# Kernel optimization log

Measured on AMD Instinct MI355X. Metric: run time of the kernel, lower is better.

The kernel has to match this reference:

```python
import math
import jax, jax.numpy as jnp
import numpy as np

B, S, D, H = 4, 2048, 1024, 16
HD = D // H  # head_dim = 64
EPS = 1e-6
LOG2_E = 1.442695041


def setup_inputs() -> dict:
    key = jax.random.key(0)
    ks = jax.random.split(key, 8)
    return {
        "inputs_q": jax.random.normal(ks[0], (B, S, D), dtype=jnp.float32),
        "Wq": jax.random.normal(ks[1], (D, D), dtype=jnp.float32) * 0.02,
        "Wk": jax.random.normal(ks[2], (D, D), dtype=jnp.float32) * 0.02,
        "Wv": jax.random.normal(ks[3], (D, D), dtype=jnp.float32) * 0.02,
        "Wo": jax.random.normal(ks[4], (D, D), dtype=jnp.float32) * 0.02,
        "q_ln_scale": jnp.ones((HD,), dtype=jnp.float32),
        "k_ln_scale": jnp.ones((HD,), dtype=jnp.float32),
        "per_dim_scale": jax.random.normal(ks[5], (HD,), dtype=jnp.float32) * 0.1,
        "patch_mask": jnp.zeros((B, S), dtype=bool),
    }


def _rope(x, position):
    # x: [B, S, H, HD], position: [B, S]
    half = HD // 2
    fraction = 2.0 * jnp.arange(half, dtype=jnp.float32) / HD
    timescale = 1.0 * (10000.0 / 1.0) ** fraction            # [half]
    sinusoid = position[:, :, None, None].astype(jnp.float32) / timescale[None, None, None, :]
    sin, cos = jnp.sin(sinusoid), jnp.cos(sinusoid)
    first, second = jnp.split(x, 2, axis=-1)
    return jnp.concatenate([first * cos - second * sin,
                            second * cos + first * sin], axis=-1)


def _rms_norm(x, scale):
    var = jnp.mean(jnp.square(x), axis=-1, keepdims=True)
    return x * jax.lax.rsqrt(var + EPS) * scale


def reference(inputs_q, Wq, Wk, Wv, Wo, q_ln_scale, k_ln_scale, per_dim_scale, patch_mask):
    b, s, d = inputs_q.shape
    # QKV projections (nn.Linear, no bias): y = x @ W.T
    q = (inputs_q @ Wq.T).reshape(b, s, H, HD)
    k = (inputs_q @ Wk.T).reshape(b, s, H, HD)
    v = (inputs_q @ Wv.T).reshape(b, s, H, HD)

    num_masked = jnp.sum(patch_mask.astype(jnp.int32), axis=-1)  # [B]
    # decode_cache=None => next_index = 0
    position = jnp.arange(s, dtype=jnp.int32)[None, :] - num_masked[:, None]  # [B, S]

    q = _rope(q, position)
    k = _rope(k, position)

    q = _rms_norm(q, q_ln_scale)
    k = _rms_norm(k, k_ln_scale)

    # per-dim scale
    q = q * (LOG2_E / math.sqrt(HD) * jax.nn.softplus(per_dim_scale))

    # causal + prefix-padding mask: [B, 1, S, S]
    q_idx = jnp.arange(s)[None, None, :, None]
    kv_idx = jnp.arange(s)[None, None, None, :]
    mask = (q_idx >= kv_idx) & (kv_idx >= num_masked[:, None, None, None])

    scores = jnp.einsum("bqhd,bkhd->bhqk", q, k)
    neg = -jnp.finfo(scores.dtype).max / 2
    scores = jnp.where(mask, scores, neg)
    attn = jax.nn.softmax(scores, axis=-1)
    x = jnp.einsum("bhqk,bkhd->bqhd", attn, v).reshape(b, s, d)
    return x @ Wo.T
```

## Files before the change

### kernel.cpp

```cpp
#include <hip/hip_runtime.h>
#include <cstdint>
#include <cstddef>

#define BB 4
#define SS 2048
#define DD 1024
#define HH 16

typedef __bf16 bf16;
typedef __bf16 bf16x8 __attribute__((ext_vector_type(8)));
typedef __bf16 bf16x4 __attribute__((ext_vector_type(4)));
typedef float f32x4 __attribute__((ext_vector_type(4)));
typedef unsigned int u32;

typedef __attribute__((address_space(1))) const void* as1_cvoid;
typedef __attribute__((address_space(3))) void* as3_void;

__device__ __forceinline__ void gload_lds16(const void* g, void* l) {
  __builtin_amdgcn_global_load_lds((as1_cvoid)g, (as3_void)l, 16, 0, 0);
}

__global__ void mask_count_kernel(const unsigned char* __restrict__ mask, int* __restrict__ nm) {
  int wid = threadIdx.x >> 6, lane = threadIdx.x & 63;
  if (wid >= BB) return;
  int s = 0;
  for (int i = lane; i < SS; i += 64) s += (mask[wid * SS + i] != 0) ? 1 : 0;
#pragma unroll
  for (int m = 1; m < 64; m <<= 1) s += __shfl_xor(s, m);
  if (lane == 0) nm[wid] = s;
}

__global__ void cvt_kernel(const float* __restrict__ src, bf16* __restrict__ dst, int n4) {
  int stride = gridDim.x * blockDim.x;
  for (int i = blockIdx.x * blockDim.x + threadIdx.x; i < n4; i += stride) {
    float4 v = ((const float4*)src)[i];
    bf16x4 o;
    o[0] = (bf16)v.x; o[1] = (bf16)v.y; o[2] = (bf16)v.z; o[3] = (bf16)v.w;
    ((bf16x4*)dst)[i] = o;
  }
}

__global__ void sincos_table_kernel(const int* __restrict__ nm, float2* __restrict__ tbl) {
  int g = blockIdx.x * 256 + threadIdx.x;
  int j = g & 31;
  int idx = g >> 5;
  int b = idx >> 11, s = idx & 2047;
  int pos = s - nm[b];
  float inv_ts = __expf((float)j * (-9.210340371976184f / 32.0f));
  float sn, cs;
  sincosf((float)pos * inv_ts, &sn, &cs);
  tbl[g] = make_float2(cs, sn);
}

__global__ void __launch_bounds__(256) gemm_qkv_kernel(
    const bf16* __restrict__ A, const bf16* __restrict__ Wq, const bf16* __restrict__ Wk,
    const bf16* __restrict__ Wv, const float* __restrict__ qls, const float* __restrict__ kls,
    const float* __restrict__ pds, const float2* __restrict__ tbl,
    bf16* __restrict__ Qp, bf16* __restrict__ Kp, bf16* __restrict__ Vt) {
  __shared__ __align__(16) char smem[4 * 64 * 72 * 2];
  bf16* Ab = (bf16*)smem;
  bf16* Bb = (bf16*)(smem + 8192);
  const int tid = threadIdx.x;
  const int wid = tid >> 6, lane = tid & 63;
  const int lr = lane & 15, lg = lane >> 4;
  const int K = DD;
  const int nx = 24;
  const int cpx = gridDim.x >> 3;
  const int lid = (blockIdx.x & 7) * cpx + (blockIdx.x >> 3);
  const int m0 = (lid / nx) * 128;
  const int ntile = lid % nx;
  const int which = ntile >> 3;
  const int n0 = (ntile & 7) * 128;
  const bf16* Bm = which == 0 ? Wq : (which == 1 ? Wk : Wv);
  const int wm = (wid >> 1) * 64, wn = (wid & 1) * 64;
  f32x4 acc[4][4] = {};
  for (int k0 = 0; k0 < K; k0 += 32) {
    __syncthreads();
#pragma unroll
    for (int i = 0; i < 2; ++i) {
      int o = (wid * 2 + i) * 1024 + lane * 16;
      int row = o >> 6;
      int ke = (o & 63) >> 1;
      gload_lds16(A + (size_t)(m0 + row) * K + k0 + ke, (char*)Ab + o);
      gload_lds16(Bm + (size_t)(n0 + row) * K + k0 + ke, (char*)Bb + o);
    }
    __syncthreads();
    bf16x8 af[4], bf_[4];
#pragma unroll
    for (int i = 0; i < 4; ++i) af[i] = *(const bf16x8*)&Ab[(wm + i * 16 + lr) * 32 + lg * 8];
#pragma unroll
    for (int j = 0; j < 4; ++j) bf_[j] = *(const bf16x8*)&Bb[(wn + j * 16 + lr) * 32 + lg * 8];
#pragma unroll
    for (int i = 0; i < 4; ++i)
#pragma unroll
      for (int j = 0; j < 4; ++j)
        acc[i][j] = __builtin_amdgcn_mfma_f32_16x16x32_bf16(af[i], bf_[j], acc[i][j], 0, 0, 0);
  }
  const int b = m0 >> 11;
  const int s0g = m0 & 2047;
  const int hq = n0 >> 6;
  if (which < 2) {
    float scj[4];
#pragma unroll
    for (int j = 0; j < 4; ++j) {
      int d = j * 16 + lr;
      scj[j] = (which == 0) ? qls[d] * 0.26017112262570096f * log1pf(__expf(pds[d]))
                            : kls[d];
    }
    bf16* Out = which == 0 ? Qp : Kp;
    const int h = hq + (wn >> 6);
    const size_t base = (size_t)(b * 16 + h) * SS;
#pragma unroll
    for (int i = 0; i < 4; ++i)
#pragma unroll
      for (int r = 0; r < 4; ++r) {
        int srow = s0g + wm + i * 16 + lg * 4 + r;
        const float2* trow = tbl + ((size_t)(b * SS + srow) << 5);
        float2 t0 = trow[lr], t1 = trow[16 + lr];
        float a0 = acc[i][0][r], a1 = acc[i][1][r], a2 = acc[i][2][r], a3 = acc[i][3][r];
        float n0_ = a0 * t0.x - a2 * t0.y;
        float n2_ = a2 * t0.x + a0 * t0.y;
        float n1_ = a1 * t1.x - a3 * t1.y;
        float n3_ = a3 * t1.x + a1 * t1.y;
        float ssum = n0_ * n0_ + n1_ * n1_ + n2_ * n2_ + n3_ * n3_;
        ssum += __shfl_xor(ssum, 1);
        ssum += __shfl_xor(ssum, 2);
        ssum += __shfl_xor(ssum, 4);
        ssum += __shfl_xor(ssum, 8);
        float rinv = rsqrtf(ssum * (1.0f / 64.0f) + 1e-6f);
        bf16* orow = Out + (base + srow) * 64;
        orow[lr]      = (bf16)(n0_ * rinv * scj[0]);
        orow[16 + lr] = (bf16)(n1_ * rinv * scj[1]);
        orow[32 + lr] = (bf16)(n2_ * rinv * scj[2]);
        orow[48 + lr] = (bf16)(n3_ * rinv * scj[3]);
      }
  } else {
    __syncthreads();
    bf16* tw = (bf16*)smem + wid * 64 * 72;
#pragma unroll
    for (int i = 0; i < 4; ++i)
#pragma unroll
      for (int j = 0; j < 4; ++j)
#pragma unroll
        for (int r = 0; r < 4; ++r)
          tw[(j * 16 + lr) * 72 + i * 16 + lg * 4 + r] = (bf16)acc[i][j][r];
    __syncthreads();
    int d = tid >> 2, sc = (tid & 3) * 16;
#pragma unroll
    for (int w = 0; w < 4; ++w) {
      int rh = w >> 1, hh = w & 1;
      const bf16* ts = (const bf16*)smem + w * 64 * 72 + d * 72 + sc;
      bf16x8 v0 = *(const bf16x8*)ts;
      bf16x8 v1 = *(const bf16x8*)(ts + 8);
      size_t vo = ((size_t)((b * 16 + hq + hh) * 64 + d)) * SS + s0g + rh * 64 + sc;
      *(bf16x8*)(Vt + vo) = v0;
      *(bf16x8*)(Vt + vo + 8) = v1;
    }
  }
}

__global__ void __launch_bounds__(256) gemm_bt_kernel(const bf16* __restrict__ A,
                                                      const bf16* __restrict__ Bm,
                                                      float* __restrict__ Cout,
                                                      int M, int N, int K) {
  __shared__ bf16 Ab[128 * 32];
  __shared__ bf16 Bb[128 * 32];
  const int tid = threadIdx.x;
  const int wid = tid >> 6, lane = tid & 63;
  const int lr = lane & 15, lg = lane >> 4;
  const int nx = N >> 7;
  const int cpx = gridDim.x >> 3;
  const int lid = (blockIdx.x & 7) * cpx + (blockIdx.x >> 3);
  const int m0 = (lid / nx) * 128, n0 = (lid % nx) * 128;
  const int wm = (wid >> 1) * 64, wn = (wid & 1) * 64;
  f32x4 acc[4][4] = {};
  for (int k0 = 0; k0 < K; k0 += 32) {
    __syncthreads();
#pragma unroll
    for (int i = 0; i < 2; ++i) {
      int o = (wid * 2 + i) * 1024 + lane * 16;
      int row = o >> 6;
      int ke = (o & 63) >> 1;
      gload_lds16(A + (size_t)(m0 + row) * K + k0 + ke, (char*)Ab + o);
      gload_lds16(Bm + (size_t)(n0 + row) * K + k0 + ke, (char*)Bb + o);
    }
    __syncthreads();
    bf16x8 af[4], bf_[4];
#pragma unroll
    for (int i = 0; i < 4; ++i) af[i] = *(const bf16x8*)&Ab[(wm + i * 16 + lr) * 32 + lg * 8];
#pragma unroll
    for (int j = 0; j < 4; ++j) bf_[j] = *(const bf16x8*)&Bb[(wn + j * 16 + lr) * 32 + lg * 8];
#pragma unroll
    for (int i = 0; i < 4; ++i)
#pragma unroll
      for (int j = 0; j < 4; ++j)
        acc[i][j] = __builtin_amdgcn_mfma_f32_16x16x32_bf16(af[i], bf_[j], acc[i][j], 0, 0, 0);
  }
#pragma unroll
  for (int i = 0; i < 4; ++i)
#pragma unroll
    for (int j = 0; j < 4; ++j)
#pragma unroll
      for (int r = 0; r < 4; ++r) {
        int row = m0 + wm + i * 16 + lg * 4 + r;
        int col = n0 + wn + j * 16 + lr;
        Cout[(size_t)row * N + col] = acc[i][j][r];
      }
}

__global__ void __launch_bounds__(256, 2) flash_kernel(
    const bf16* __restrict__ Qp, const bf16* __restrict__ Kp, const bf16* __restrict__ Vt,
    bf16* __restrict__ O, const int* __restrict__ nm) {
  __shared__ bf16 Kb[2][64 * 64];
  __shared__ bf16 Vb[64 * 64];
  __shared__ u32 Pl[4][16][36];
  const int bh = blockIdx.x & 63;
  const int px = blockIdx.x >> 6;
  const int xA = 31 - px, xB = px;
  const int b = bh >> 4, h = bh & 15;
  const int tid = threadIdx.x;
  const int wid = tid >> 6, lane = tid & 63;
  const int lr = lane & 15, lg = lane >> 4;
  const int nmb = nm[b];
  const int wqA = xA * 64 + wid * 16;
  const int wqB = xB * 64 + wid * 16;
  const int nt = xA + 1;

  bf16x8 qfA[2], qfB[2];
#pragma unroll
  for (int kh = 0; kh < 2; ++kh) {
    qfA[kh] = *(const bf16x8*)(Qp + ((size_t)bh * SS + wqA + lr) * 64 + kh * 32 + lg * 8);
    qfB[kh] = *(const bf16x8*)(Qp + ((size_t)bh * SS + wqB + lr) * 64 + kh * 32 + lg * 8);
  }

  float mA = -1e30f, lA = 0.f, mB = -1e30f, lB = 0.f;
  f32x4 oA[4] = {}, oB[4] = {};

  auto STAGE_K = [&](int bi, int t) {
    const int kv0 = t * 64;
#pragma unroll
    for (int i = 0; i < 2; ++i) {
      int o = i * 4096 + tid * 16;
      int row = o >> 7;
      int c16 = ((o >> 4) & 7) ^ (row & 7);
      gload_lds16(Kp + ((size_t)bh * SS + kv0 + row) * 64 + c16 * 8, (char*)Kb[bi] + o);
    }
  };
  auto STAGE_V = [&](int t) {
    const int kv0 = t * 64;
#pragma unroll
    for (int i = 0; i < 2; ++i) {
      int o = i * 4096 + tid * 16;
      int row = o >> 7;
      int c16 = ((o >> 4) & 7) ^ (row & 7);
      gload_lds16(Vt + ((size_t)bh * 64 + row) * SS + kv0 + c16 * 8, (char*)Vb + o);
    }
  };

  STAGE_K(0, 0);
  STAGE_V(0);
  __syncthreads();
  int buf = 0;
  for (int t = 0; t < nt; ++t) {
    const int kv0 = t * 64;
    if (t + 1 < nt) STAGE_K(buf ^ 1, t + 1);
    const bool actB = (t <= xB);
    bf16x8 pbA[2], pbB[2];
    f32x4 sA[4], sB[4];

    __builtin_amdgcn_s_setprio(1);
#pragma unroll
    for (int j = 0; j < 4; ++j) {
      int row = j * 16 + lr;
      const char* kbase = (const char*)Kb[buf] + row * 128;
      bf16x8 kf0 = *(const bf16x8*)(kbase + ((lg ^ (row & 7)) << 4));
      bf16x8 kf1 = *(const bf16x8*)(kbase + (((4 + lg) ^ (row & 7)) << 4));
      f32x4 z = {};
      z = __builtin_amdgcn_mfma_f32_16x16x32_bf16(kf0, qfA[0], z, 0, 0, 0);
      z = __builtin_amdgcn_mfma_f32_16x16x32_bf16(kf1, qfA[1], z, 0, 0, 0);
      sA[j] = z;
      if (actB) {
        f32x4 z2 = {};
        z2 = __builtin_amdgcn_mfma_f32_16x16x32_bf16(kf0, qfB[0], z2, 0, 0, 0);
        z2 = __builtin_amdgcn_mfma_f32_16x16x32_bf16(kf1, qfB[1], z2, 0, 0, 0);
        sB[j] = z2;
      }
    }
    __builtin_amdgcn_s_setprio(0);

    auto SOFTMAX = [&](f32x4* s, float& m_r, float& l_pp, f32x4* oacc, bf16x8* pb,
                       int xS, int wqS) {
      if (t == xS) {
        int qr = wqS + lr;
#pragma unroll
        for (int j = 0; j < 4; ++j) {
          int kvb = kv0 + j * 16 + lg * 4;
#pragma unroll
          for (int r = 0; r < 4; ++r)
            if (kvb + r > qr) s[j][r] = -1e30f;
        }
      }
      if (kv0 < nmb) {
#pragma unroll
        for (int j = 0; j < 4; ++j) {
          int kvb = kv0 + j * 16 + lg * 4;
#pragma unroll
          for (int r = 0; r < 4; ++r)
            if (kvb + r < nmb) s[j][r] = -1e30f;
        }
      }
      float t0 = fmaxf(fmaxf(s[0][0], s[0][1]), s[0][2]);
      float t1 = fmaxf(fmaxf(s[0][3], s[1][0]), s[1][1]);
      float t2 = fmaxf(fmaxf(s[1][2], s[1][3]), s[2][0]);
      float t3 = fmaxf(fmaxf(s[2][1], s[2][2]), s[2][3]);
      float t4 = fmaxf(fmaxf(s[3][0], s[3][1]), s[3][2]);
      float t5 = fmaxf(fmaxf(t0, t1), s[3][3]);
      float pm = fmaxf(fmaxf(t2, t3), fmaxf(t4, t5));
      if (!__all(pm - m_r <= 8.f)) {
        pm = fmaxf(pm, __shfl_xor(pm, 16));
        pm = fmaxf(pm, __shfl_xor(pm, 32));
        float mn = fmaxf(m_r, pm);
        float scl = exp2f(m_r - mn);
        m_r = mn;
        l_pp *= scl;
        f32x4 sv = {scl, scl, scl, scl};
#pragma unroll
        for (int jd = 0; jd < 4; ++jd) oacc[jd] *= sv;
      }
      const float mloc = m_r;
      float lp = l_pp;
#pragma unroll
      for (int j = 0; j < 4; ++j) {
        float p0 = exp2f(s[j][0] - mloc), p1 = exp2f(s[j][1] - mloc);
        float p2 = exp2f(s[j][2] - mloc), p3 = exp2f(s[j][3] - mloc);
        lp += (p0 + p1) + (p2 + p3);
        union { bf16 hx[4]; uint2 u2; } pk;
        pk.hx[0] = (bf16)p0; pk.hx[1] = (bf16)p1;
        pk.hx[2] = (bf16)p2; pk.hx[3] = (bf16)p3;
        *(uint2*)&Pl[wid][lr][j * 8 + lg * 2] = pk.u2;
      }
      l_pp = lp;
#pragma unroll
      for (int kh = 0; kh < 2; ++kh) pb[kh] = *(const bf16x8*)&Pl[wid][lr][kh * 16 + lg * 4];
    };

    SOFTMAX(sA, mA, lA, oA, pbA, xA, wqA);
    if (actB) SOFTMAX(sB, mB, lB, oB, pbB, xB, wqB);

    if (t > 0) {
      if (t + 1 < nt)
        asm volatile("s_waitcnt vmcnt(2)" ::: "memory");
      else
        asm volatile("s_waitcnt vmcnt(0)" ::: "memory");
      __builtin_amdgcn_s_barrier();
      __builtin_amdgcn_sched_barrier(0);
    }
    __builtin_amdgcn_s_setprio(1);
#pragma unroll
    for (int jd = 0; jd < 4; ++jd) {
      int row = jd * 16 + lr;
      const char* vbase = (const char*)Vb + row * 128;
      bf16x8 va0 = *(const bf16x8*)(vbase + ((lg ^ (row & 7)) << 4));
      bf16x8 va1 = *(const bf16x8*)(vbase + (((4 + lg) ^ (row & 7)) << 4));
      oA[jd] = __builtin_amdgcn_mfma_f32_16x16x32_bf16(va0, pbA[0], oA[jd], 0, 0, 0);
      oA[jd] = __builtin_amdgcn_mfma_f32_16x16x32_bf16(va1, pbA[1], oA[jd], 0, 0, 0);
      if (actB) {
        oB[jd] = __builtin_amdgcn_mfma_f32_16x16x32_bf16(va0, pbB[0], oB[jd], 0, 0, 0);
        oB[jd] = __builtin_amdgcn_mfma_f32_16x16x32_bf16(va1, pbB[1], oB[jd], 0, 0, 0);
      }
    }
    __builtin_amdgcn_s_setprio(0);
    __syncthreads();
    if (t + 1 < nt) STAGE_V(t + 1);
    buf ^= 1;
  }
#pragma unroll
  for (int st = 0; st < 2; ++st) {
    float l = st == 0 ? lA : lB;
    const f32x4* oacc = st == 0 ? oA : oB;
    int wq = st == 0 ? wqA : wqB;
    l += __shfl_xor(l, 16);
    l += __shfl_xor(l, 32);
    float invl = 1.0f / l;
    size_t rowoff = ((size_t)b * SS + wq + lr) * DD + h * 64;
#pragma unroll
    for (int jd = 0; jd < 4; ++jd) {
      f32x4 ov = oacc[jd] * invl;
      bf16x4 hv;
      hv[0] = (bf16)ov[0]; hv[1] = (bf16)ov[1]; hv[2] = (bf16)ov[2]; hv[3] = (bf16)ov[3];
      *(bf16x4*)(O + rowoff + jd * 16 + lg * 4) = hv;
    }
  }
}

extern "C" void kernel_launch(void* const* d_in, const int* in_sizes, int n_in,
                              void* d_out, int out_size, void* d_ws, size_t ws_size,
                              hipStream_t stream) {
  const float* X = (const float*)d_in[0];
  const float* Wq = (const float*)d_in[1];
  const float* Wk = (const float*)d_in[2];
  const float* Wv = (const float*)d_in[3];
  const float* Wo = (const float*)d_in[4];
  const float* qls = (const float*)d_in[5];
  const float* kls = (const float*)d_in[6];
  const float* pds = (const float*)d_in[7];
  const unsigned char* mask = (const unsigned char*)d_in[8];

  char* ws = (char*)d_ws;
  size_t off = 0;
  auto alloc = [&](size_t bytes) {
    char* p = ws + off;
    off += (bytes + 255) & ~(size_t)255;
    return p;
  };
  const size_t NTOK = (size_t)BB * SS;
  int* nm = (int*)alloc(16);
  bf16* Xb = (bf16*)alloc(NTOK * DD * 2);
  bf16* Wqb = (bf16*)alloc((size_t)DD * DD * 2);
  bf16* Wkb = (bf16*)alloc((size_t)DD * DD * 2);
  bf16* Wvb = (bf16*)alloc((size_t)DD * DD * 2);
  bf16* Wob = (bf16*)alloc((size_t)DD * DD * 2);
  bf16* Qp = (bf16*)alloc(NTOK * DD * 2);
  bf16* Kp = (bf16*)alloc(NTOK * DD * 2);
  bf16* Vt = (bf16*)alloc(NTOK * DD * 2);
  float2* tbl = (float2*)alloc(NTOK * 32 * sizeof(float2));
  bf16* Oat = Xb;

  mask_count_kernel<<<1, 256, 0, stream>>>(mask, nm);
  cvt_kernel<<<1024, 256, 0, stream>>>(X, Xb, (int)(NTOK * DD / 4));
  cvt_kernel<<<256, 256, 0, stream>>>(Wq, Wqb, DD * DD / 4);
  cvt_kernel<<<256, 256, 0, stream>>>(Wk, Wkb, DD * DD / 4);
  cvt_kernel<<<256, 256, 0, stream>>>(Wv, Wvb, DD * DD / 4);
  cvt_kernel<<<256, 256, 0, stream>>>(Wo, Wob, DD * DD / 4);
  sincos_table_kernel<<<1024, 256, 0, stream>>>(nm, tbl);

  gemm_qkv_kernel<<<(int)(NTOK / 128) * 24, 256, 0, stream>>>(Xb, Wqb, Wkb, Wvb, qls, kls, pds,
                                                              tbl, Qp, Kp, Vt);
  flash_kernel<<<1024, 256, 0, stream>>>(Qp, Kp, Vt, Oat, nm);
  gemm_bt_kernel<<<(int)(NTOK / 128) * (DD / 128), 256, 0, stream>>>(Oat, Wob, (float*)d_out,
                                                                     (int)NTOK, DD, DD);
}
```

Baseline: 199.8 us.

## Merge weight conversions into one launch, XOR-swizzle P scratch, precompute flash addresses

```diff
diff --git a/kernel.cpp b/kernel.cpp
--- a/kernel.cpp
+++ b/kernel.cpp
@@ -33,6 +33,22 @@
 __global__ void cvt_kernel(const float* __restrict__ src, bf16* __restrict__ dst, int n4) {
   int stride = gridDim.x * blockDim.x;
   for (int i = blockIdx.x * blockDim.x + threadIdx.x; i < n4; i += stride) {
+    float4 v = ((const float4*)src)[i];
+    bf16x4 o;
+    o[0] = (bf16)v.x; o[1] = (bf16)v.y; o[2] = (bf16)v.z; o[3] = (bf16)v.w;
+    ((bf16x4*)dst)[i] = o;
+  }
+}
+
+__global__ void cvt4_kernel(const float* __restrict__ W0, const float* __restrict__ W1,
+                            const float* __restrict__ W2, const float* __restrict__ W3,
+                            bf16* __restrict__ D0, bf16* __restrict__ D1,
+                            bf16* __restrict__ D2, bf16* __restrict__ D3) {
+  int which = blockIdx.x >> 8;
+  const float* src = which == 0 ? W0 : which == 1 ? W1 : which == 2 ? W2 : W3;
+  bf16* dst = which == 0 ? D0 : which == 1 ? D1 : which == 2 ? D2 : D3;
+  const int n4 = DD * DD / 4;
+  for (int i = (blockIdx.x & 255) * 256 + threadIdx.x; i < n4; i += 65536) {
     float4 v = ((const float4*)src)[i];
     bf16x4 o;
     o[0] = (bf16)v.x; o[1] = (bf16)v.y; o[2] = (bf16)v.z; o[3] = (bf16)v.w;
@@ -213,7 +229,7 @@
     bf16* __restrict__ O, const int* __restrict__ nm) {
   __shared__ bf16 Kb[2][64 * 64];
   __shared__ bf16 Vb[64 * 64];
-  __shared__ u32 Pl[4][16][36];
+  __shared__ u32 Pl[4][16][32];
   const int bh = blockIdx.x & 63;
   const int px = blockIdx.x >> 6;
   const int xA = 31 - px, xB = px;
@@ -221,11 +237,27 @@
   const int tid = threadIdx.x;
   const int wid = tid >> 6, lane = tid & 63;
   const int lr = lane & 15, lg = lane >> 4;
+  const int sw = (lr & 7) << 2;
   const int nmb = nm[b];
   const int wqA = xA * 64 + wid * 16;
   const int wqB = xB * 64 + wid * 16;
   const int nt = xA + 1;
 
+  const int koffA = lr * 128 + ((lg ^ (lr & 7)) << 4);
+  const int koffB = lr * 128 + (((4 + lg) ^ (lr & 7)) << 4);
+  const int o0 = tid * 16, o1 = 4096 + tid * 16;
+  const int r0 = o0 >> 7, r1 = o1 >> 7;
+  const int c0 = ((o0 >> 4) & 7) ^ (r0 & 7), c1 = ((o1 >> 4) & 7) ^ (r1 & 7);
+  const bf16* kg0 = Kp + (size_t)bh * (SS * 64) + r0 * 64 + c0 * 8;
+  const bf16* kg1 = Kp + (size_t)bh * (SS * 64) + r1 * 64 + c1 * 8;
+  const bf16* vg0 = Vt + (size_t)bh * (SS * 64) + (size_t)r0 * SS + c0 * 8;
+  const bf16* vg1 = Vt + (size_t)bh * (SS * 64) + (size_t)r1 * SS + c1 * 8;
+  char* kl0 = (char*)&Kb[0][0] + o0;
+  char* kl1 = (char*)&Kb[0][0] + o1;
+  char* vl0 = (char*)Vb + o0;
+  char* vl1 = (char*)Vb + o1;
+  u32* plw = &Pl[wid][lr][0];
+
   bf16x8 qfA[2], qfB[2];
 #pragma unroll
   for (int kh = 0; kh < 2; ++kh) {
@@ -237,24 +269,12 @@
   f32x4 oA[4] = {}, oB[4] = {};
 
   auto STAGE_K = [&](int bi, int t) {
-    const int kv0 = t * 64;
-#pragma unroll
-    for (int i = 0; i < 2; ++i) {
-      int o = i * 4096 + tid * 16;
-      int row = o >> 7;
-      int c16 = ((o >> 4) & 7) ^ (row & 7);
-      gload_lds16(Kp + ((size_t)bh * SS + kv0 + row) * 64 + c16 * 8, (char*)Kb[bi] + o);
-    }
+    gload_lds16(kg0 + (size_t)t * 4096, kl0 + bi * 8192);
+    gload_lds16(kg1 + (size_t)t * 4096, kl1 + bi * 8192);
   };
   auto STAGE_V = [&](int t) {
-    const int kv0 = t * 64;
-#pragma unroll
-    for (int i = 0; i < 2; ++i) {
-      int o = i * 4096 + tid * 16;
-      int row = o >> 7;
-      int c16 = ((o >> 4) & 7) ^ (row & 7);
-      gload_lds16(Vt + ((size_t)bh * 64 + row) * SS + kv0 + c16 * 8, (char*)Vb + o);
-    }
+    gload_lds16(vg0 + t * 64, vl0);
+    gload_lds16(vg1 + t * 64, vl1);
   };
 
   STAGE_K(0, 0);
@@ -265,16 +285,14 @@
     const int kv0 = t * 64;
     if (t + 1 < nt) STAGE_K(buf ^ 1, t + 1);
     const bool actB = (t <= xB);
-    bf16x8 pbA[2], pbB[2];
     f32x4 sA[4], sB[4];
 
+    const char* kbb = (const char*)&Kb[0][0] + buf * 8192;
     __builtin_amdgcn_s_setprio(1);
 #pragma unroll
     for (int j = 0; j < 4; ++j) {
-      int row = j * 16 + lr;
-      const char* kbase = (const char*)Kb[buf] + row * 128;
-      bf16x8 kf0 = *(const bf16x8*)(kbase + ((lg ^ (row & 7)) << 4));
-      bf16x8 kf1 = *(const bf16x8*)(kbase + (((4 + lg) ^ (row & 7)) << 4));
+      bf16x8 kf0 = *(const bf16x8*)(kbb + koffA + j * 2048);
+      bf16x8 kf1 = *(const bf16x8*)(kbb + koffB + j * 2048);
       f32x4 z = {};
       z = __builtin_amdgcn_mfma_f32_16x16x32_bf16(kf0, qfA[0], z, 0, 0, 0);
       z = __builtin_amdgcn_mfma_f32_16x16x32_bf16(kf1, qfA[1], z, 0, 0, 0);
@@ -337,13 +355,15 @@
         union { bf16 hx[4]; uint2 u2; } pk;
         pk.hx[0] = (bf16)p0; pk.hx[1] = (bf16)p1;
         pk.hx[2] = (bf16)p2; pk.hx[3] = (bf16)p3;
-        *(uint2*)&Pl[wid][lr][j * 8 + lg * 2] = pk.u2;
+        *(uint2*)&plw[(j * 8 + lg * 2) ^ sw] = pk.u2;
       }
       l_pp = lp;
 #pragma unroll
-      for (int kh = 0; kh < 2; ++kh) pb[kh] = *(const bf16x8*)&Pl[wid][lr][kh * 16 + lg * 4];
+      for (int kh = 0; kh < 2; ++kh)
+        pb[kh] = *(const bf16x8*)&plw[(kh * 16 + lg * 4) ^ sw];
     };
 
+    bf16x8 pbA[2], pbB[2];
     SOFTMAX(sA, mA, lA, oA, pbA, xA, wqA);
     if (actB) SOFTMAX(sB, mB, lB, oB, pbB, xB, wqB);
 
@@ -358,10 +378,8 @@
     __builtin_amdgcn_s_setprio(1);
 #pragma unroll
     for (int jd = 0; jd < 4; ++jd) {
-      int row = jd * 16 + lr;
-      const char* vbase = (const char*)Vb + row * 128;
-      bf16x8 va0 = *(const bf16x8*)(vbase + ((lg ^ (row & 7)) << 4));
-      bf16x8 va1 = *(const bf16x8*)(vbase + (((4 + lg) ^ (row & 7)) << 4));
+      bf16x8 va0 = *(const bf16x8*)((const char*)Vb + koffA + jd * 2048);
+      bf16x8 va1 = *(const bf16x8*)((const char*)Vb + koffB + jd * 2048);
       oA[jd] = __builtin_amdgcn_mfma_f32_16x16x32_bf16(va0, pbA[0], oA[jd], 0, 0, 0);
       oA[jd] = __builtin_amdgcn_mfma_f32_16x16x32_bf16(va1, pbA[1], oA[jd], 0, 0, 0);
       if (actB) {
@@ -428,10 +446,7 @@
 
   mask_count_kernel<<<1, 256, 0, stream>>>(mask, nm);
   cvt_kernel<<<1024, 256, 0, stream>>>(X, Xb, (int)(NTOK * DD / 4));
-  cvt_kernel<<<256, 256, 0, stream>>>(Wq, Wqb, DD * DD / 4);
-  cvt_kernel<<<256, 256, 0, stream>>>(Wk, Wkb, DD * DD / 4);
-  cvt_kernel<<<256, 256, 0, stream>>>(Wv, Wvb, DD * DD / 4);
-  cvt_kernel<<<256, 256, 0, stream>>>(Wo, Wob, DD * DD / 4);
+  cvt4_kernel<<<1024, 256, 0, stream>>>(Wq, Wk, Wv, Wo, Wqb, Wkb, Wvb, Wob);
   sincos_table_kernel<<<1024, 256, 0, stream>>>(nm, tbl);
 
   gemm_qkv_kernel<<<(int)(NTOK / 128) * 24, 256, 0, stream>>>(Xb, Wqb, Wkb, Wvb, qls, kls, pds,
```

New measurement: 197.2 us. No clear change (-1.3%).
